# Optimization experiments

Measured on AMD Instinct MI355X. Metric: run time of the kernel, lower is better.

Reference implementation:

```python
import jax, jax.numpy as jnp
import numpy as np

N_NODES = 10000
N_EDGES = 160000
D_IN = 512
D_OUT = 512


def setup_inputs() -> dict:
    key = jax.random.key(0)
    k_x, k_e, k_wl, k_wr = jax.random.split(key, 4)
    x = jax.random.normal(k_x, (N_NODES, D_IN), dtype=jnp.float32)
    edge_index = jax.random.randint(k_e, (2, N_EDGES), 0, N_NODES, dtype=jnp.int64)
    scale = 1.0 / np.sqrt(D_IN)
    W_l = jax.random.normal(k_wl, (D_IN, D_OUT), dtype=jnp.float32) * scale
    W_r = jax.random.normal(k_wr, (D_IN, D_OUT), dtype=jnp.float32) * scale
    b = jnp.zeros((D_OUT,), dtype=jnp.float32)
    return {"x": x, "edge_index": edge_index, "W_l": W_l, "W_r": W_r, "b": b}


def reference(x, edge_index, W_l, W_r, b):
    # dropout p=0.0 -> identity
    src = edge_index[0]  # message sources (x_j)
    dst = edge_index[1]  # aggregation targets (i)
    n = x.shape[0]
    # mean neighbor aggregation: scatter-add messages, divide by in-degree
    msg = x[src]                                   # [E, D_in]
    agg = jax.ops.segment_sum(msg, dst, num_segments=n)        # [N, D_in]
    deg = jax.ops.segment_sum(jnp.ones((src.shape[0],), x.dtype), dst, num_segments=n)
    mean = agg / jnp.maximum(deg, 1.0)[:, None]
    # SAGEConv: lin_l(aggregated) + lin_r(root), bias in lin_l
    h = mean @ W_l + b + x @ W_r                   # [N, D_out]
    # Swish activation
    return h * jax.nn.sigmoid(h)
```

## Files before the change

### kernel.cpp

```cpp
#include <hip/hip_runtime.h>
#include <cstdint>
#include <cstddef>

typedef unsigned short ushort_t;
typedef __attribute__((ext_vector_type(8))) short short8;
typedef __attribute__((ext_vector_type(4))) float float4_;

#define GLOBAL_AS __attribute__((address_space(1)))
#define LDS_AS    __attribute__((address_space(3)))

#define D_FEAT 512
#define KDIM   1024
#define CAP    80

__device__ __forceinline__ ushort_t f2bf(float f) {
    union { float f; unsigned int i; } v; v.f = f;
    unsigned int x = v.i;
    unsigned int r = (x + 0x7fffu + ((x >> 16) & 1u)) >> 16;
    return (ushort_t)r;
}
__device__ __forceinline__ float bfbits_lo(unsigned int u) {
    union { unsigned int i; float f; } v; v.i = u << 16; return v.f;
}
__device__ __forceinline__ float bfbits_hi(unsigned int u) {
    union { unsigned int i; float f; } v; v.i = u & 0xffff0000u; return v.f;
}

__global__ __launch_bounds__(256) void prep_kernel(
    const float* __restrict__ Wl, const float* __restrict__ Wr,
    const float* __restrict__ x, ushort_t* __restrict__ BT,
    ushort_t* __restrict__ xb, int* __restrict__ cnt, int cnt_n, int nchunks) {
    int b = blockIdx.x;
    int t = threadIdx.x;
    if (b < 128) {
        int zi = b * 256 + t;
        if (zi < cnt_n) cnt[zi] = 0;
        __shared__ float tile[64][68];
        int kb = (b & 15) * 64, nb = (b >> 4) * 64;
#pragma unroll
        for (int ph = 0; ph < 4; ++ph) {
            int f = t * 4 + ph * 1024;
            int k = f >> 6, n = f & 63;
            int gk = kb + k;
            const float* W = (gk < 512) ? (Wl + (size_t)gk * 512 + nb + n)
                                        : (Wr + (size_t)(gk - 512) * 512 + nb + n);
            *(float4*)&tile[k][n] = *(const float4*)W;
        }
        __syncthreads();
#pragma unroll
        for (int ph = 0; ph < 4; ++ph) {
            int f = t * 4 + ph * 1024;
            int n = f >> 6, k = f & 63;
            ushort_t tmp[4];
#pragma unroll
            for (int j = 0; j < 4; ++j) tmp[j] = f2bf(tile[k + j][n]);
            *(uint2*)&BT[(size_t)(nb + n) * KDIM + kb + k] = *(const uint2*)tmp;
        }
    } else {
        int idx = (b - 128) * 256 + t;
        if (idx >= nchunks) return;
        int row = idx >> 7;
        int c = (idx & 127) << 2;
        float4 v = *(const float4*)&x[(size_t)row * D_FEAT + c];
        ushort_t o[4] = {f2bf(v.x), f2bf(v.y), f2bf(v.z), f2bf(v.w)};
        *(uint2*)&xb[(size_t)row * D_FEAT + c] = *(const uint2*)o;
    }
}

__global__ __launch_bounds__(256) void bucket_kernel(
    const int* __restrict__ ei, int* __restrict__ cnt,
    int* __restrict__ colbuf, int E) {
    int e = blockIdx.x * 256 + threadIdx.x;
    if (e >= E) return;
    int d = ei[E + e];
    int p = atomicAdd(&cnt[d], 1);
    if (p < CAP) colbuf[(size_t)d * CAP + p] = ei[e];
}

__global__ __launch_bounds__(256) void agg_kernel(
    const ushort_t* __restrict__ xb, ushort_t* __restrict__ mb,
    const int* __restrict__ cnt, const int* __restrict__ colbuf, int n) {
    int w = threadIdx.x >> 6, l = threadIdx.x & 63;
    int node = blockIdx.x * 4 + w;
    if (node >= n) return;
    int f = l << 3;
    const ushort_t* gsrc = xb + f;
    const int* bucket = colbuf + (size_t)node * CAP;
    float acc[8] = {0.f, 0.f, 0.f, 0.f, 0.f, 0.f, 0.f, 0.f};
    int deg = cnt[node];
    int e = deg < CAP ? deg : CAP;
    int j = 0;
    for (; j + 3 < e; j += 4) {
        int s0 = bucket[j], s1 = bucket[j + 1];
        int s2 = bucket[j + 2], s3 = bucket[j + 3];
        uint4 v0 = *(const uint4*)(gsrc + (size_t)s0 * D_FEAT);
        uint4 v1 = *(const uint4*)(gsrc + (size_t)s1 * D_FEAT);
        uint4 v2 = *(const uint4*)(gsrc + (size_t)s2 * D_FEAT);
        uint4 v3 = *(const uint4*)(gsrc + (size_t)s3 * D_FEAT);
        acc[0] += bfbits_lo(v0.x); acc[1] += bfbits_hi(v0.x);
        acc[2] += bfbits_lo(v0.y); acc[3] += bfbits_hi(v0.y);
        acc[4] += bfbits_lo(v0.z); acc[5] += bfbits_hi(v0.z);
        acc[6] += bfbits_lo(v0.w); acc[7] += bfbits_hi(v0.w);
        acc[0] += bfbits_lo(v1.x); acc[1] += bfbits_hi(v1.x);
        acc[2] += bfbits_lo(v1.y); acc[3] += bfbits_hi(v1.y);
        acc[4] += bfbits_lo(v1.z); acc[5] += bfbits_hi(v1.z);
        acc[6] += bfbits_lo(v1.w); acc[7] += bfbits_hi(v1.w);
        acc[0] += bfbits_lo(v2.x); acc[1] += bfbits_hi(v2.x);
        acc[2] += bfbits_lo(v2.y); acc[3] += bfbits_hi(v2.y);
        acc[4] += bfbits_lo(v2.z); acc[5] += bfbits_hi(v2.z);
        acc[6] += bfbits_lo(v2.w); acc[7] += bfbits_hi(v2.w);
        acc[0] += bfbits_lo(v3.x); acc[1] += bfbits_hi(v3.x);
        acc[2] += bfbits_lo(v3.y); acc[3] += bfbits_hi(v3.y);
        acc[4] += bfbits_lo(v3.z); acc[5] += bfbits_hi(v3.z);
        acc[6] += bfbits_lo(v3.w); acc[7] += bfbits_hi(v3.w);
    }
    for (; j < e; ++j) {
        int s0 = bucket[j];
        uint4 v0 = *(const uint4*)(gsrc + (size_t)s0 * D_FEAT);
        acc[0] += bfbits_lo(v0.x); acc[1] += bfbits_hi(v0.x);
        acc[2] += bfbits_lo(v0.y); acc[3] += bfbits_hi(v0.y);
        acc[4] += bfbits_lo(v0.z); acc[5] += bfbits_hi(v0.z);
        acc[6] += bfbits_lo(v0.w); acc[7] += bfbits_hi(v0.w);
    }
    float scale = 1.0f / (float)(deg > 1 ? deg : 1);
    ushort_t o[8];
#pragma unroll
    for (int k = 0; k < 8; ++k) o[k] = f2bf(acc[k] * scale);
    *(uint4*)&mb[(size_t)node * D_FEAT + f] = *(const uint4*)o;
}

__global__ __launch_bounds__(256) void gemm_kernel(
    const ushort_t* __restrict__ mb, const ushort_t* __restrict__ xb,
    const ushort_t* __restrict__ BT, const float* __restrict__ bias,
    float* __restrict__ out, int nrows) {
    __shared__ ushort_t As[128 * 32];
    __shared__ ushort_t Bs[64 * 32];
    int tile_n = blockIdx.x * 64;
    int tile_m = blockIdx.y * 128;
    int tid = threadIdx.x;
    int w = tid >> 6, l = tid & 63;
    int lm = l & 15, q = l >> 4;
    int wm = w * 32;

    float4_ acc[2][4];
#pragma unroll
    for (int i = 0; i < 2; ++i)
#pragma unroll
        for (int j = 0; j < 4; ++j) acc[i][j] = (float4_)(0.f);

    int c0 = w * 64 + l;

    for (int k0 = 0; k0 < KDIM; k0 += 32) {
        const ushort_t* Asrc = (k0 < 512) ? mb : xb;
        int kk = k0 & 511;
#pragma unroll
        for (int ph = 0; ph < 2; ++ph) {
            int c = c0 + ph * 256;
            int row = c >> 2;
            int koff = (c & 3) << 3;
            const ushort_t* gp = Asrc + (size_t)(tile_m + row) * D_FEAT + kk + koff;
            __builtin_amdgcn_global_load_lds(
                (const GLOBAL_AS unsigned int*)gp,
                (LDS_AS unsigned int*)&As[c * 8], 16, 0, 0);
        }
        {
            int c = c0;
            int row = c >> 2;
            int koff = (c & 3) << 3;
            const ushort_t* gq = BT + (size_t)(tile_n + row) * KDIM + k0 + koff;
            __builtin_amdgcn_global_load_lds(
                (const GLOBAL_AS unsigned int*)gq,
                (LDS_AS unsigned int*)&Bs[c * 8], 16, 0, 0);
        }
        __syncthreads();

        short8 a[2], b[4];
#pragma unroll
        for (int i = 0; i < 2; ++i) {
            int row = wm + i * 16 + lm;
            a[i] = *(const short8*)&As[row * 32 + q * 8];
        }
#pragma unroll
        for (int j = 0; j < 4; ++j) {
            int col = j * 16 + lm;
            b[j] = *(const short8*)&Bs[col * 32 + q * 8];
        }
#pragma unroll
        for (int i = 0; i < 2; ++i)
#pragma unroll
            for (int j = 0; j < 4; ++j)
                acc[i][j] = __builtin_amdgcn_mfma_f32_16x16x32_bf16(
                    a[i], b[j], acc[i][j], 0, 0, 0);
        __syncthreads();
    }

#pragma unroll
    for (int j = 0; j < 4; ++j) {
        int gcol = tile_n + j * 16 + lm;
        float bv = bias[gcol];
#pragma unroll
        for (int i = 0; i < 2; ++i) {
#pragma unroll
            for (int r = 0; r < 4; ++r) {
                int grow = tile_m + wm + i * 16 + q * 4 + r;
                if (grow < nrows) {
                    float h = acc[i][j][r] + bv;
                    float sw = h / (1.f + __expf(-h));
                    out[(size_t)grow * D_FEAT + gcol] = sw;
                }
            }
        }
    }
}

extern "C" void kernel_launch(void* const* d_in, const int* in_sizes, int n_in,
                              void* d_out, int out_size, void* d_ws, size_t ws_size,
                              hipStream_t stream) {
    const float* x    = (const float*)d_in[0];
    const int*   ei   = (const int*)d_in[1];
    const float* Wl   = (const float*)d_in[2];
    const float* Wr   = (const float*)d_in[3];
    const float* bias = (const float*)d_in[4];
    float* out = (float*)d_out;

    const int N = in_sizes[0] / D_FEAT;
    const int E = in_sizes[1] / 2;
    const int MT = (N + 127) / 128;
    const int M_PAD = MT * 128;

    char* ws = (char*)d_ws;
    size_t off = 0;
    auto take = [&](size_t bytes) -> char* {
        char* p = ws + off;
        off += (bytes + 255) & ~(size_t)255;
        return p;
    };
    ushort_t* xb     = (ushort_t*)take((size_t)M_PAD * D_FEAT * 2);
    ushort_t* mb     = (ushort_t*)take((size_t)M_PAD * D_FEAT * 2);
    ushort_t* BT     = (ushort_t*)take((size_t)D_FEAT * KDIM * 2);
    int*      cnt    = (int*)take((size_t)M_PAD * 4);
    int*      colbuf = (int*)take((size_t)M_PAD * CAP * 4);

    int nchunks = N * (D_FEAT / 4);
    int cb = (nchunks + 255) / 256;
    prep_kernel<<<128 + cb, 256, 0, stream>>>(Wl, Wr, x, BT, xb, cnt, M_PAD, nchunks);

    int eb = (E + 255) / 256;
    bucket_kernel<<<eb, 256, 0, stream>>>(ei, cnt, colbuf, E);

    agg_kernel<<<(N + 3) / 4, 256, 0, stream>>>(xb, mb, cnt, colbuf, N);

    gemm_kernel<<<dim3(D_FEAT / 64, MT), 256, 0, stream>>>(mb, xb, BT, bias, out, N);
}
```

Baseline: 144.1 us.

## Fuse all stages into one cooperative persistent kernel with grid syncs

Merges the prep, bucketing, aggregation and GEMM kernels into one cooperative launch. The stages are separated by grid.sync and each stage uses grid-stride loops over a persistent grid capped at 1024 blocks. The weight tile is also converted to bf16 before it is staged in LDS, so LDS use is shared across stages. This is meant to remove the overhead of launching and draining several kernels, but it adds grid-wide barrier costs and limits the parallelism of each stage to the resident blocks. The GEMM stage has 632 tiles spread over at most 1024 blocks.

```diff
diff --git a/kernel.cpp b/kernel.cpp
--- a/kernel.cpp
+++ b/kernel.cpp
@@ -1,6 +1,9 @@
 #include <hip/hip_runtime.h>
+#include <hip/hip_cooperative_groups.h>
 #include <cstdint>
 #include <cstddef>
+
+namespace cg = cooperative_groups;
 
 typedef unsigned short ushort_t;
 typedef __attribute__((ext_vector_type(8))) short short8;
@@ -26,16 +29,20 @@
     union { unsigned int i; float f; } v; v.i = u & 0xffff0000u; return v.f;
 }
 
-__global__ __launch_bounds__(256) void prep_kernel(
+__global__ __launch_bounds__(256) void mega_kernel(
     const float* __restrict__ Wl, const float* __restrict__ Wr,
-    const float* __restrict__ x, ushort_t* __restrict__ BT,
-    ushort_t* __restrict__ xb, int* __restrict__ cnt, int cnt_n, int nchunks) {
+    const float* __restrict__ x, const int* __restrict__ ei,
+    const float* __restrict__ bias, ushort_t* __restrict__ BT,
+    ushort_t* __restrict__ xb, ushort_t* __restrict__ mb,
+    int* __restrict__ cnt, int* __restrict__ colbuf,
+    float* __restrict__ out, int N, int E, int M_PAD, int G) {
+    __shared__ ushort_t smem[6144];
+    cg::grid_group grid = cg::this_grid();
     int b = blockIdx.x;
     int t = threadIdx.x;
+
     if (b < 128) {
-        int zi = b * 256 + t;
-        if (zi < cnt_n) cnt[zi] = 0;
-        __shared__ float tile[64][68];
+        ushort_t (*tile)[72] = (ushort_t (*)[72])smem;
         int kb = (b & 15) * 64, nb = (b >> 4) * 64;
 #pragma unroll
         for (int ph = 0; ph < 4; ++ph) {
@@ -44,7 +51,9 @@
             int gk = kb + k;
             const float* W = (gk < 512) ? (Wl + (size_t)gk * 512 + nb + n)
                                         : (Wr + (size_t)(gk - 512) * 512 + nb + n);
-            *(float4*)&tile[k][n] = *(const float4*)W;
+            float4 v = *(const float4*)W;
+            ushort_t o[4] = {f2bf(v.x), f2bf(v.y), f2bf(v.z), f2bf(v.w)};
+            *(uint2*)&tile[k][n] = *(const uint2*)o;
         }
         __syncthreads();
 #pragma unroll
@@ -53,160 +62,163 @@
             int n = f >> 6, k = f & 63;
             ushort_t tmp[4];
 #pragma unroll
-            for (int j = 0; j < 4; ++j) tmp[j] = f2bf(tile[k + j][n]);
+            for (int j = 0; j < 4; ++j) tmp[j] = tile[k + j][n];
             *(uint2*)&BT[(size_t)(nb + n) * KDIM + kb + k] = *(const uint2*)tmp;
         }
+    } else if (b < 168) {
+        int zi = (b - 128) * 256 + t;
+        if (zi < M_PAD) cnt[zi] = 0;
     } else {
-        int idx = (b - 128) * 256 + t;
-        if (idx >= nchunks) return;
-        int row = idx >> 7;
-        int c = (idx & 127) << 2;
-        float4 v = *(const float4*)&x[(size_t)row * D_FEAT + c];
-        ushort_t o[4] = {f2bf(v.x), f2bf(v.y), f2bf(v.z), f2bf(v.w)};
-        *(uint2*)&xb[(size_t)row * D_FEAT + c] = *(const uint2*)o;
-    }
-}
-
-__global__ __launch_bounds__(256) void bucket_kernel(
-    const int* __restrict__ ei, int* __restrict__ cnt,
-    int* __restrict__ colbuf, int E) {
-    int e = blockIdx.x * 256 + threadIdx.x;
-    if (e >= E) return;
-    int d = ei[E + e];
-    int p = atomicAdd(&cnt[d], 1);
-    if (p < CAP) colbuf[(size_t)d * CAP + p] = ei[e];
-}
-
-__global__ __launch_bounds__(256) void agg_kernel(
-    const ushort_t* __restrict__ xb, ushort_t* __restrict__ mb,
-    const int* __restrict__ cnt, const int* __restrict__ colbuf, int n) {
-    int w = threadIdx.x >> 6, l = threadIdx.x & 63;
-    int node = blockIdx.x * 4 + w;
-    if (node >= n) return;
-    int f = l << 3;
-    const ushort_t* gsrc = xb + f;
-    const int* bucket = colbuf + (size_t)node * CAP;
-    float acc[8] = {0.f, 0.f, 0.f, 0.f, 0.f, 0.f, 0.f, 0.f};
-    int deg = cnt[node];
-    int e = deg < CAP ? deg : CAP;
-    int j = 0;
-    for (; j + 3 < e; j += 4) {
-        int s0 = bucket[j], s1 = bucket[j + 1];
-        int s2 = bucket[j + 2], s3 = bucket[j + 3];
-        uint4 v0 = *(const uint4*)(gsrc + (size_t)s0 * D_FEAT);
-        uint4 v1 = *(const uint4*)(gsrc + (size_t)s1 * D_FEAT);
-        uint4 v2 = *(const uint4*)(gsrc + (size_t)s2 * D_FEAT);
-        uint4 v3 = *(const uint4*)(gsrc + (size_t)s3 * D_FEAT);
-        acc[0] += bfbits_lo(v0.x); acc[1] += bfbits_hi(v0.x);
-        acc[2] += bfbits_lo(v0.y); acc[3] += bfbits_hi(v0.y);
-        acc[4] += bfbits_lo(v0.z); acc[5] += bfbits_hi(v0.z);
-        acc[6] += bfbits_lo(v0.w); acc[7] += bfbits_hi(v0.w);
-        acc[0] += bfbits_lo(v1.x); acc[1] += bfbits_hi(v1.x);
-        acc[2] += bfbits_lo(v1.y); acc[3] += bfbits_hi(v1.y);
-        acc[4] += bfbits_lo(v1.z); acc[5] += bfbits_hi(v1.z);
-        acc[6] += bfbits_lo(v1.w); acc[7] += bfbits_hi(v1.w);
-        acc[0] += bfbits_lo(v2.x); acc[1] += bfbits_hi(v2.x);
-        acc[2] += bfbits_lo(v2.y); acc[3] += bfbits_hi(v2.y);
-        acc[4] += bfbits_lo(v2.z); acc[5] += bfbits_hi(v2.z);
-        acc[6] += bfbits_lo(v2.w); acc[7] += bfbits_hi(v2.w);
-        acc[0] += bfbits_lo(v3.x); acc[1] += bfbits_hi(v3.x);
-        acc[2] += bfbits_lo(v3.y); acc[3] += bfbits_hi(v3.y);
-        acc[4] += bfbits_lo(v3.z); acc[5] += bfbits_hi(v3.z);
-        acc[6] += bfbits_lo(v3.w); acc[7] += bfbits_hi(v3.w);
-    }
-    for (; j < e; ++j) {
-        int s0 = bucket[j];
-        uint4 v0 = *(const uint4*)(gsrc + (size_t)s0 * D_FEAT);
-        acc[0] += bfbits_lo(v0.x); acc[1] += bfbits_hi(v0.x);
-        acc[2] += bfbits_lo(v0.y); acc[3] += bfbits_hi(v0.y);
-        acc[4] += bfbits_lo(v0.z); acc[5] += bfbits_hi(v0.z);
-        acc[6] += bfbits_lo(v0.w); acc[7] += bfbits_hi(v0.w);
-    }
-    float scale = 1.0f / (float)(deg > 1 ? deg : 1);
-    ushort_t o[8];
-#pragma unroll
-    for (int k = 0; k < 8; ++k) o[k] = f2bf(acc[k] * scale);
-    *(uint4*)&mb[(size_t)node * D_FEAT + f] = *(const uint4*)o;
-}
-
-__global__ __launch_bounds__(256) void gemm_kernel(
-    const ushort_t* __restrict__ mb, const ushort_t* __restrict__ xb,
-    const ushort_t* __restrict__ BT, const float* __restrict__ bias,
-    float* __restrict__ out, int nrows) {
-    __shared__ ushort_t As[128 * 32];
-    __shared__ ushort_t Bs[64 * 32];
-    int tile_n = blockIdx.x * 64;
-    int tile_m = blockIdx.y * 128;
-    int tid = threadIdx.x;
-    int w = tid >> 6, l = tid & 63;
-    int lm = l & 15, q = l >> 4;
-    int wm = w * 32;
-
-    float4_ acc[2][4];
-#pragma unroll
-    for (int i = 0; i < 2; ++i)
-#pragma unroll
-        for (int j = 0; j < 4; ++j) acc[i][j] = (float4_)(0.f);
-
-    int c0 = w * 64 + l;
-
-    for (int k0 = 0; k0 < KDIM; k0 += 32) {
-        const ushort_t* Asrc = (k0 < 512) ? mb : xb;
-        int kk = k0 & 511;
-#pragma unroll
-        for (int ph = 0; ph < 2; ++ph) {
-            int c = c0 + ph * 256;
-            int row = c >> 2;
-            int koff = (c & 3) << 3;
-            const ushort_t* gp = Asrc + (size_t)(tile_m + row) * D_FEAT + kk + koff;
-            __builtin_amdgcn_global_load_lds(
-                (const GLOBAL_AS unsigned int*)gp,
-                (LDS_AS unsigned int*)&As[c * 8], 16, 0, 0);
-        }
-        {
-            int c = c0;
-            int row = c >> 2;
-            int koff = (c & 3) << 3;
-            const ushort_t* gq = BT + (size_t)(tile_n + row) * KDIM + k0 + koff;
-            __builtin_amdgcn_global_load_lds(
-                (const GLOBAL_AS unsigned int*)gq,
-                (LDS_AS unsigned int*)&Bs[c * 8], 16, 0, 0);
-        }
-        __syncthreads();
-
-        short8 a[2], b[4];
-#pragma unroll
-        for (int i = 0; i < 2; ++i) {
-            int row = wm + i * 16 + lm;
-            a[i] = *(const short8*)&As[row * 32 + q * 8];
-        }
-#pragma unroll
-        for (int j = 0; j < 4; ++j) {
-            int col = j * 16 + lm;
-            b[j] = *(const short8*)&Bs[col * 32 + q * 8];
-        }
-#pragma unroll
-        for (int i = 0; i < 2; ++i)
-#pragma unroll
-            for (int j = 0; j < 4; ++j)
-                acc[i][j] = __builtin_amdgcn_mfma_f32_16x16x32_bf16(
-                    a[i], b[j], acc[i][j], 0, 0, 0);
-        __syncthreads();
-    }
-
-#pragma unroll
-    for (int j = 0; j < 4; ++j) {
-        int gcol = tile_n + j * 16 + lm;
-        float bv = bias[gcol];
-#pragma unroll
-        for (int i = 0; i < 2; ++i) {
-#pragma unroll
-            for (int r = 0; r < 4; ++r) {
-                int grow = tile_m + wm + i * 16 + q * 4 + r;
-                if (grow < nrows) {
-                    float h = acc[i][j][r] + bv;
-                    float sw = h / (1.f + __expf(-h));
-                    out[(size_t)grow * D_FEAT + gcol] = sw;
+        int nch = N * (D_FEAT / 4);
+        int stride = (G - 168) * 256;
+        for (int idx = (b - 168) * 256 + t; idx < nch; idx += stride) {
+            int row = idx >> 7;
+            int c = (idx & 127) << 2;
+            float4 v = *(const float4*)&x[(size_t)row * D_FEAT + c];
+            ushort_t o[4] = {f2bf(v.x), f2bf(v.y), f2bf(v.z), f2bf(v.w)};
+            *(uint2*)&xb[(size_t)row * D_FEAT + c] = *(const uint2*)o;
+        }
+    }
+    grid.sync();
+
+    for (int e = b * 256 + t; e < E; e += G * 256) {
+        int d = ei[E + e];
+        int p = atomicAdd(&cnt[d], 1);
+        if (p < CAP) colbuf[(size_t)d * CAP + p] = ei[e];
+    }
+    grid.sync();
+
+    {
+        int w = t >> 6, l = t & 63;
+        int f = l << 3;
+        const ushort_t* gsrc = xb + f;
+        for (int node = b * 4 + w; node < N; node += G * 4) {
+            const int* bucket = colbuf + (size_t)node * CAP;
+            float acc[8] = {0.f, 0.f, 0.f, 0.f, 0.f, 0.f, 0.f, 0.f};
+            int deg = cnt[node];
+            int e = deg < CAP ? deg : CAP;
+            int j = 0;
+            for (; j + 3 < e; j += 4) {
+                int s0 = bucket[j], s1 = bucket[j + 1];
+                int s2 = bucket[j + 2], s3 = bucket[j + 3];
+                uint4 v0 = *(const uint4*)(gsrc + (size_t)s0 * D_FEAT);
+                uint4 v1 = *(const uint4*)(gsrc + (size_t)s1 * D_FEAT);
+                uint4 v2 = *(const uint4*)(gsrc + (size_t)s2 * D_FEAT);
+                uint4 v3 = *(const uint4*)(gsrc + (size_t)s3 * D_FEAT);
+                acc[0] += bfbits_lo(v0.x); acc[1] += bfbits_hi(v0.x);
+                acc[2] += bfbits_lo(v0.y); acc[3] += bfbits_hi(v0.y);
+                acc[4] += bfbits_lo(v0.z); acc[5] += bfbits_hi(v0.z);
+                acc[6] += bfbits_lo(v0.w); acc[7] += bfbits_hi(v0.w);
+                acc[0] += bfbits_lo(v1.x); acc[1] += bfbits_hi(v1.x);
+                acc[2] += bfbits_lo(v1.y); acc[3] += bfbits_hi(v1.y);
+                acc[4] += bfbits_lo(v1.z); acc[5] += bfbits_hi(v1.z);
+                acc[6] += bfbits_lo(v1.w); acc[7] += bfbits_hi(v1.w);
+                acc[0] += bfbits_lo(v2.x); acc[1] += bfbits_hi(v2.x);
+                acc[2] += bfbits_lo(v2.y); acc[3] += bfbits_hi(v2.y);
+                acc[4] += bfbits_lo(v2.z); acc[5] += bfbits_hi(v2.z);
+                acc[6] += bfbits_lo(v2.w); acc[7] += bfbits_hi(v2.w);
+                acc[0] += bfbits_lo(v3.x); acc[1] += bfbits_hi(v3.x);
+                acc[2] += bfbits_lo(v3.y); acc[3] += bfbits_hi(v3.y);
+                acc[4] += bfbits_lo(v3.z); acc[5] += bfbits_hi(v3.z);
+                acc[6] += bfbits_lo(v3.w); acc[7] += bfbits_hi(v3.w);
+            }
+            for (; j < e; ++j) {
+                int s0 = bucket[j];
+                uint4 v0 = *(const uint4*)(gsrc + (size_t)s0 * D_FEAT);
+                acc[0] += bfbits_lo(v0.x); acc[1] += bfbits_hi(v0.x);
+                acc[2] += bfbits_lo(v0.y); acc[3] += bfbits_hi(v0.y);
+                acc[4] += bfbits_lo(v0.z); acc[5] += bfbits_hi(v0.z);
+                acc[6] += bfbits_lo(v0.w); acc[7] += bfbits_hi(v0.w);
+            }
+            float scale = 1.0f / (float)(deg > 1 ? deg : 1);
+            ushort_t o[8];
+#pragma unroll
+            for (int k = 0; k < 8; ++k) o[k] = f2bf(acc[k] * scale);
+            *(uint4*)&mb[(size_t)node * D_FEAT + f] = *(const uint4*)o;
+        }
+    }
+    grid.sync();
+
+    {
+        ushort_t* As = smem;
+        ushort_t* Bs = smem + 4096;
+        int w = t >> 6, l = t & 63;
+        int lm = l & 15, q = l >> 4;
+        int wm = w * 32;
+        int c0 = w * 64 + l;
+        int ntiles = (D_FEAT / 64) * (M_PAD / 128);
+
+        for (int tile_i = b; tile_i < ntiles; tile_i += G) {
+            int tile_n = (tile_i & 7) * 64;
+            int tile_m = (tile_i >> 3) * 128;
+
+            float4_ acc[2][4];
+#pragma unroll
+            for (int i = 0; i < 2; ++i)
+#pragma unroll
+                for (int j = 0; j < 4; ++j) acc[i][j] = (float4_)(0.f);
+
+            for (int k0 = 0; k0 < KDIM; k0 += 32) {
+                const ushort_t* Asrc = (k0 < 512) ? mb : xb;
+                int kk = k0 & 511;
+#pragma unroll
+                for (int ph = 0; ph < 2; ++ph) {
+                    int c = c0 + ph * 256;
+                    int row = c >> 2;
+                    int koff = (c & 3) << 3;
+                    const ushort_t* gp =
+                        Asrc + (size_t)(tile_m + row) * D_FEAT + kk + koff;
+                    __builtin_amdgcn_global_load_lds(
+                        (const GLOBAL_AS unsigned int*)gp,
+                        (LDS_AS unsigned int*)&As[c * 8], 16, 0, 0);
+                }
+                {
+                    int c = c0;
+                    int row = c >> 2;
+                    int koff = (c & 3) << 3;
+                    const ushort_t* gq =
+                        BT + (size_t)(tile_n + row) * KDIM + k0 + koff;
+                    __builtin_amdgcn_global_load_lds(
+                        (const GLOBAL_AS unsigned int*)gq,
+                        (LDS_AS unsigned int*)&Bs[c * 8], 16, 0, 0);
+                }
+                __syncthreads();
+
+                short8 a[2], bb[4];
+#pragma unroll
+                for (int i = 0; i < 2; ++i) {
+                    int row = wm + i * 16 + lm;
+                    a[i] = *(const short8*)&As[row * 32 + q * 8];
+                }
+#pragma unroll
+                for (int j = 0; j < 4; ++j) {
+                    int col = j * 16 + lm;
+                    bb[j] = *(const short8*)&Bs[col * 32 + q * 8];
+                }
+#pragma unroll
+                for (int i = 0; i < 2; ++i)
+#pragma unroll
+                    for (int j = 0; j < 4; ++j)
+                        acc[i][j] = __builtin_amdgcn_mfma_f32_16x16x32_bf16(
+                            a[i], bb[j], acc[i][j], 0, 0, 0);
+                __syncthreads();
+            }
+
+#pragma unroll
+            for (int j = 0; j < 4; ++j) {
+                int gcol = tile_n + j * 16 + lm;
+                float bv = bias[gcol];
+#pragma unroll
+                for (int i = 0; i < 2; ++i) {
+#pragma unroll
+                    for (int r = 0; r < 4; ++r) {
+                        int grow = tile_m + wm + i * 16 + q * 4 + r;
+                        if (grow < N) {
+                            float h = acc[i][j][r] + bv;
+                            float sw = h / (1.f + __expf(-h));
+                            out[(size_t)grow * D_FEAT + gcol] = sw;
+                        }
+                    }
                 }
             }
         }
@@ -223,10 +235,10 @@
     const float* bias = (const float*)d_in[4];
     float* out = (float*)d_out;
 
-    const int N = in_sizes[0] / D_FEAT;
-    const int E = in_sizes[1] / 2;
-    const int MT = (N + 127) / 128;
-    const int M_PAD = MT * 128;
+    int N = in_sizes[0] / D_FEAT;
+    int E = in_sizes[1] / 2;
+    int MT = (N + 127) / 128;
+    int M_PAD = MT * 128;
 
     char* ws = (char*)d_ws;
     size_t off = 0;
@@ -241,14 +253,15 @@
     int*      cnt    = (int*)take((size_t)M_PAD * 4);
     int*      colbuf = (int*)take((size_t)M_PAD * CAP * 4);
 
-    int nchunks = N * (D_FEAT / 4);
-    int cb = (nchunks + 255) / 256;
-    prep_kernel<<<128 + cb, 256, 0, stream>>>(Wl, Wr, x, BT, xb, cnt, M_PAD, nchunks);
-
-    int eb = (E + 255) / 256;
-    bucket_kernel<<<eb, 256, 0, stream>>>(ei, cnt, colbuf, E);
-
-    agg_kernel<<<(N + 3) / 4, 256, 0, stream>>>(xb, mb, cnt, colbuf, N);
-
-    gemm_kernel<<<dim3(D_FEAT / 64, MT), 256, 0, stream>>>(mb, xb, BT, bias, out, N);
-}
+    int maxb = 0;
+    hipOccupancyMaxActiveBlocksPerMultiprocessor(&maxb, mega_kernel, 256, 0);
+    if (maxb < 1) maxb = 1;
+    int G = maxb * 256;
+    if (G > 1024) G = 1024;
+
+    void* args[] = {(void*)&Wl, (void*)&Wr, (void*)&x, (void*)&ei, (void*)&bias,
+                    (void*)&BT, (void*)&xb, (void*)&mb, (void*)&cnt,
+                    (void*)&colbuf, (void*)&out, (void*)&N, (void*)&E,
+                    (void*)&M_PAD, (void*)&G};
+    hipLaunchCooperativeKernel(mega_kernel, dim3(G), dim3(256), args, 0, stream);
+}
```

Result: slower. 364.9 us (+153.2%).
